# Kernel optimization log

Hardware: AMD Instinct MI355X
Metric: run time of the kernel (lower is better)

Reference implementation:

```python
import jax, jax.numpy as jnp
import numpy as np

B, S, D, F, E, CAP = 4, 2048, 1024, 4096, 8, 320


def setup_inputs() -> dict:
    key = jax.random.key(0)
    k1, k2, k3, k4 = jax.random.split(key, 4)
    return {
        "hidden_states": jax.random.normal(k1, (B, S, D), dtype=jnp.float32),
        "router_w": jax.random.normal(k2, (D, E), dtype=jnp.float32) * 0.02,
        "wi": jax.random.normal(k3, (E, D, F), dtype=jnp.float32) * 0.02,
        "wo": jax.random.normal(k4, (E, F, D), dtype=jnp.float32) * 0.02,
    }


def reference(hidden_states, router_w, wi, wo):
    # ---- Router (Switch top-1 with per-sequence expert capacity) ----
    b, s, d = hidden_states.shape
    e = router_w.shape[1]
    logits = hidden_states.astype(jnp.float32) @ router_w          # [B,S,E]
    probs = jax.nn.softmax(logits, axis=-1)                        # [B,S,E]
    expert_idx = jnp.argmax(probs, axis=-1)                        # [B,S]
    onehot = jax.nn.one_hot(expert_idx, e, dtype=jnp.int32)        # [B,S,E]
    priority = jnp.cumsum(onehot, axis=1)                          # cumsum over seq dim (dim=-2)
    keep = onehot * (priority <= CAP).astype(jnp.int32)            # capacity-masked router_mask

    # slot of each token within its chosen expert (0-based)
    slot = jnp.take_along_axis(priority, expert_idx[..., None], axis=-1)[..., 0] - 1  # [B,S]
    valid = slot < CAP                                             # dropped tokens exceed capacity
    slot_sc = jnp.where(valid, slot, CAP)                          # out-of-range -> dropped by scatter

    b_ar = jnp.broadcast_to(jnp.arange(b)[:, None], (b, s))
    s_ar = jnp.broadcast_to(jnp.arange(s)[None, :], (b, s))
    dispatch = jnp.zeros((b, e, CAP), jnp.int32).at[b_ar, expert_idx, slot_sc].set(
        s_ar.astype(jnp.int32), mode="drop")                       # [B,E,CAP] token index per slot
    slot_used = jnp.zeros((b, e, CAP), bool).at[b_ar, expert_idx, slot_sc].set(
        valid, mode="drop")                                        # [B,E,CAP]

    # ---- Dispatch: gather tokens into [B,E,CAP,D] ----
    xg = jax.vmap(lambda xb, ib: xb[ib])(hidden_states, dispatch)  # [B,E,CAP,D]

    # ---- Per-expert dense FFN (grouped GEMM) ----
    hg = jax.nn.relu(jnp.einsum("becd,edf->becf", xg, wi))         # [B,E,CAP,F]
    yg = jnp.einsum("becf,efd->becd", hg, wo)                      # [B,E,CAP,D]

    # ---- Combine: scatter expert outputs back; unrouted tokens keep input ----
    idx_back = jnp.where(slot_used, dispatch, s)                   # out-of-range -> dropped
    next_states = jax.vmap(
        lambda xb, ib, yb: xb.at[ib.reshape(-1)].set(yb.reshape(-1, d), mode="drop")
    )(hidden_states, idx_back, yg)                                 # [B,S,D]

    max_prob = jnp.max(probs, axis=-1, keepdims=True)              # [B,S,1]
    out = max_prob * next_states
    expert_index_out = jnp.argmax(keep, axis=-1)                   # [B,S] (0 for dropped tokens)
    return out, logits, expert_index_out
```

## Files before the change

### kernel.cpp

```cpp
#include <hip/hip_runtime.h>
#include <hip/hip_bf16.h>
#include <stdint.h>

#define B_ 4
#define S_ 2048
#define D_ 1024
#define F_ 4096
#define E_ 8
#define CAP_ 320
#define BS_ (B_*S_)
#define MPE 1280

typedef unsigned short u16;
typedef __attribute__((ext_vector_type(8))) short bf16x8;
typedef __attribute__((ext_vector_type(4))) float f32x4;
typedef __attribute__((ext_vector_type(4))) unsigned short u16x4;
typedef __attribute__((ext_vector_type(8))) unsigned short u16x8;

__device__ __forceinline__ u16 f2bf(float f) {
  union { float f; uint32_t u; } v; v.f = f;
  uint32_t r = (v.u + 0x7FFFu + ((v.u >> 16) & 1u)) >> 16;
  return (u16)r;
}

__device__ __forceinline__ void gload16(const void* g, void* l) {
  __builtin_amdgcn_global_load_lds(
      (const __attribute__((address_space(1))) uint32_t*)g,
      (__attribute__((address_space(3))) uint32_t*)l, 16, 0, 0);
}

__device__ __forceinline__ void transpose_block(
    const float* __restrict__ W, u16* __restrict__ WT,
    const int K, const int N, const int bid, void* ldsraw)
{
  float (*tile)[65] = (float(*)[65])ldsraw;
  const int tk = K >> 7, tn = N >> 6;
  const int e = bid / (tk * tn), r = bid % (tk * tn);
  const int k0 = (r / tn) << 7, n0 = (r % tn) << 6;
  const float* We = W + (size_t)e * K * N;
  u16* WTe = WT + (size_t)e * N * K;
  const int t = threadIdx.x;
  const int fr = t >> 2, c0 = (t & 3) * 16;
#pragma unroll
  for (int j = 0; j < 4; ++j) {
    const float4 v = *(const float4*)(We + (size_t)(k0 + fr) * N + n0 + c0 + j * 4);
    tile[fr][c0 + j*4 + 0] = v.x; tile[fr][c0 + j*4 + 1] = v.y;
    tile[fr][c0 + j*4 + 2] = v.z; tile[fr][c0 + j*4 + 3] = v.w;
  }
  __syncthreads();
  const int nr = t >> 3, kk0 = (t & 7) * 16;
  u16x8 o0, o1;
#pragma unroll
  for (int j = 0; j < 8; ++j) o0[j] = f2bf(tile[kk0 + j][nr]);
#pragma unroll
  for (int j = 0; j < 8; ++j) o1[j] = f2bf(tile[kk0 + 8 + j][nr]);
  u16* dst = WTe + (size_t)(n0 + nr) * K + k0 + kk0;
  *(u16x8*)dst = o0;
  *(u16x8*)(dst + 8) = o1;
}

__global__ __launch_bounds__(512) void transpose_kernel(
    const float* __restrict__ W, u16* __restrict__ WT, const int K, const int N)
{
  __shared__ __align__(16) float tile[128][65];
  transpose_block(W, WT, K, N, blockIdx.x, (void*)tile);
}

__global__ __launch_bounds__(512) void prep_kernel(
    const float* __restrict__ hs, const float* __restrict__ rw,
    const float* __restrict__ wi, u16* __restrict__ wT,
    float* __restrict__ logits, float* __restrict__ maxp,
    int* __restrict__ eidx, const int twiT)
{
  __shared__ __align__(16) float tile[128][65];
  if ((int)blockIdx.x < twiT) {
    transpose_block(wi, wT, D_, F_, blockIdx.x, (void*)tile);
    return;
  }
  const int wv = threadIdx.x >> 6, l = threadIdx.x & 63;
  const int token = (blockIdx.x - twiT) * 8 + wv;
  const float* row = hs + (size_t)token * D_;
  const float4* rw4 = (const float4*)rw;

  double acc0=0, acc1=0, acc2=0, acc3=0, acc4=0, acc5=0, acc6=0, acc7=0;
#pragma unroll
  for (int j = 0; j < 4; ++j) {
    const int d4 = l + j * 64;
    const float4 v = ((const float4*)row)[d4];
#pragma unroll
    for (int c = 0; c < 4; ++c) {
      const int d = d4 * 4 + c;
      const float x = (&v.x)[c];
      const float4 w0 = rw4[d * 2];
      const float4 w1 = rw4[d * 2 + 1];
      acc0 += (double)x * (double)w0.x;
      acc1 += (double)x * (double)w0.y;
      acc2 += (double)x * (double)w0.z;
      acc3 += (double)x * (double)w0.w;
      acc4 += (double)x * (double)w1.x;
      acc5 += (double)x * (double)w1.y;
      acc6 += (double)x * (double)w1.z;
      acc7 += (double)x * (double)w1.w;
    }
  }
  double acc[E_] = {acc0, acc1, acc2, acc3, acc4, acc5, acc6, acc7};
#pragma unroll
  for (int e = 0; e < E_; ++e) {
#pragma unroll
    for (int off = 32; off; off >>= 1)
      acc[e] += __shfl_xor(acc[e], off);
  }
  if (l == 0) {
    float lg[E_];
#pragma unroll
    for (int e = 0; e < E_; ++e) lg[e] = (float)acc[e];
    float lmax = lg[0]; int am = 0;
#pragma unroll
    for (int e = 1; e < E_; ++e) { if (lg[e] > lmax) { lmax = lg[e]; am = e; } }
    float sum = 0.f;
#pragma unroll
    for (int e = 0; e < E_; ++e) sum += expf(lg[e] - lmax);
#pragma unroll
    for (int e = 0; e < E_; ++e) logits[(size_t)token * E_ + e] = lg[e];
    maxp[token] = 1.0f / sum;
    eidx[token] = am;
  }
}

__global__ __launch_bounds__(256) void scan_kernel(
    const int* __restrict__ eidx, int* __restrict__ tok,
    float* __restrict__ eout, const float* __restrict__ hs,
    const float* __restrict__ maxp, float* __restrict__ out)
{
  const int b = blockIdx.x >> 3, e = blockIdx.x & 7;
  __shared__ int wsum[4];
  const int tid = threadIdx.x, wv = tid >> 6, l = tid & 63;
  for (int i = tid; i < CAP_; i += 256) tok[(b * E_ + e) * CAP_ + i] = -1;
  __syncthreads();
  int base = 0;
  for (int ch = 0; ch < S_ / 256; ++ch) {
    const int s = ch * 256 + tid;
    const bool p = (eidx[b * S_ + s] == e);
    const unsigned long long m = __ballot(p);
    const int lp = __popcll(m & ((1ULL << l) - 1ULL));
    if (l == 0) wsum[wv] = __popcll(m);
    __syncthreads();
    int pre = 0, tot = 0;
#pragma unroll
    for (int w = 0; w < 4; ++w) { if (w < wv) pre += wsum[w]; tot += wsum[w]; }
    if (p) {
      const int rank = base + pre + lp;
      if (rank < CAP_) {
        tok[(b * E_ + e) * CAP_ + rank] = s;
        eout[b * S_ + s] = (float)e;
      } else {
        eout[b * S_ + s] = 0.0f;
        const float mp = maxp[b * S_ + s];
        const float4* src = (const float4*)(hs + (size_t)(b * S_ + s) * D_);
        float4* dst = (float4*)(out + (size_t)(b * S_ + s) * D_);
        for (int j = 0; j < D_ / 4; ++j) {
          const float4 vv = src[j];
          float4 o; o.x = vv.x * mp; o.y = vv.y * mp; o.z = vv.z * mp; o.w = vv.w * mp;
          dst[j] = o;
        }
      }
    }
    base += tot;
    __syncthreads();
  }
}

__global__ __launch_bounds__(256) void gather_kernel(
    const float* __restrict__ hs, const int* __restrict__ tok,
    u16* __restrict__ Xg)
{
  const int bx = blockIdx.x;
  const int e = bx / MPE, r = bx % MPE;
  const int b = r / CAP_, c = r % CAP_;
  const int t = tok[(b * E_ + e) * CAP_ + c];
  const int d = threadIdx.x * 4;
  u16x4 o;
  if (t >= 0) {
    const float4 vv = *(const float4*)(hs + ((size_t)(b * S_ + t)) * D_ + d);
    o[0] = f2bf(vv.x); o[1] = f2bf(vv.y); o[2] = f2bf(vv.z); o[3] = f2bf(vv.w);
  } else {
    o[0] = 0; o[1] = 0; o[2] = 0; o[3] = 0;
  }
  *(u16x4*)(Xg + (size_t)bx * D_ + d) = o;
}

#define BAR() __builtin_amdgcn_s_barrier()
#define LGKMN(n) do { asm volatile("s_waitcnt lgkmcnt(" #n ")" ::: "memory"); \
                      __builtin_amdgcn_sched_barrier(0); } while (0)
#define VMW(n) asm volatile("s_waitcnt vmcnt(" #n ")" ::: "memory")

__global__ __launch_bounds__(512, 2) void moe_g1(
    const u16* __restrict__ Aall, const u16* __restrict__ Btall,
    u16* __restrict__ hgout, const int gemm_blocks,
    const float* __restrict__ Wtr, u16* __restrict__ WTtr)
{
  __shared__ __align__(16) u16 lds[49152];

#define LDA(p, h) (lds + (p) * 8192 + (h) * 4096)
#define LDB(p, h) (lds + 16384 + (p) * 16384 + (h) * 8192)

  if ((int)blockIdx.x >= gemm_blocks) {
    transpose_block(Wtr, WTtr, F_, D_, blockIdx.x - gemm_blocks, (void*)lds);
    return;
  }
  const int K = D_, NT = K >> 6, N = F_;
  const int cpx = gemm_blocks >> 3;
  const int bid = blockIdx.x;
  const int swzb = (bid & 7) * cpx + (bid >> 3);
  const int e = swzb / 160, rem = swzb % 160;
  const int m0 = (rem / 16) * 128, n0 = (rem % 16) * 256;

  const u16* Ae = Aall + (size_t)e * MPE * K;
  const u16* Be = Btall + (size_t)e * N * K;

  const int tid = threadIdx.x;
  const int wv = tid >> 6, l = tid & 63;
  const int wr = wv >> 2, wc = wv & 3;
  const int lr = l & 15, lk = l >> 4;
  const int rswz = ((lr >> 3) & 1) << 4;
  const int gs0 = tid ^ (((tid >> 5) & 1) << 1);
  const size_t goffB = (size_t)((gs0 >> 2) & 127) * K + (size_t)((gs0 & 3) * 8);
  const size_t goffA = (size_t)((gs0 >> 2) & 63) * K
                     + (size_t)(((gs0 >> 8) & 1) * 32) + (size_t)((gs0 & 3) * 8);
  const int dwoff = wv * 512;

  const u16* pA0 = Ae + (size_t)m0 * K;
  const u16* pA1 = Ae + (size_t)(m0 + 64) * K;
  const u16* pB0 = Be + (size_t)n0 * K;
  const u16* pB1 = Be + (size_t)(n0 + 128) * K;

  f32x4 acc[4][4];
#pragma unroll
  for (int i = 0; i < 4; ++i)
#pragma unroll
    for (int j = 0; j < 4; ++j) acc[i][j] = (f32x4){0.f, 0.f, 0.f, 0.f};

  bf16x8 faA[2], faB[2], fb[8];

#define STAGE_A1(dhalf, rb, tt) \
    gload16((rb) + goffA + (size_t)((tt) * 64), (dhalf) + dwoff)

#define STAGE_B1(dhalf, rb, tt) do {                                       \
    const u16* s_ = (rb) + goffB + (size_t)((tt) * 64);                    \
    gload16(s_,      (dhalf) + dwoff);                                     \
    gload16(s_ + 32, (dhalf) + 4096 + dwoff);                              \
  } while (0)

#define READ_AQ1(q, p, fa_) do {                                           \
    _Pragma("unroll")                                                      \
    for (int kk = 0; kk < 2; ++kk)                                         \
      fa_[kk] = *(const bf16x8*)&LDA(p, wr)                                \
          [(kk*64 + (q)*16 + lr)*32 + ((lk*8) ^ rswz)];                    \
  } while (0)

#define READ_B_ALL1(p) do {                                                \
    _Pragma("unroll")                                                      \
    for (int nf = 0; nf < 4; ++nf)                                         \
      _Pragma("unroll")                                                    \
      for (int kk = 0; kk < 2; ++kk)                                       \
        fb[nf*2+kk] = *(const bf16x8*)&LDB(p, wc>>1)                       \
            [(kk*128 + (wc&1)*64 + (nf>>1)*32 + (nf&1)*16 + lr)*32         \
             + ((lk*8) ^ rswz)];                                           \
  } while (0)

#define MFMA_P1(q, fa_) do {                                               \
    __builtin_amdgcn_s_setprio(1);                                         \
    _Pragma("unroll")                                                      \
    for (int nf = 0; nf < 4; ++nf)                                         \
      _Pragma("unroll")                                                    \
      for (int kk = 0; kk < 2; ++kk)                                       \
        acc[q][nf] = __builtin_amdgcn_mfma_f32_16x16x32_bf16(              \
            fa_[kk], fb[nf*2+kk], acc[q][nf], 0, 0, 0);                    \
    __builtin_amdgcn_s_setprio(0);                                         \
  } while (0)

#define DO_T1(p, pn, tc) do {                                              \
    READ_AQ1(1, p, faB);                                                   \
    if ((tc) + 1 < NT) { STAGE_A1(LDA(pn,0), pA0, (tc)+1);                 \
                         STAGE_A1(LDA(pn,1), pA1, (tc)+1); }               \
    LGKMN(2); MFMA_P1(0, faA);                                             \
    READ_AQ1(2, p, faA);                                                   \
    LGKMN(2); MFMA_P1(1, faB);                                             \
    BAR();                                                                 \
    READ_AQ1(3, p, faB);                                                   \
    if ((tc) + 2 < NT) { STAGE_B1(LDB(p,0), pB0, (tc)+2);                  \
                         STAGE_B1(LDB(p,1), pB1, (tc)+2); }                \
    LGKMN(2); MFMA_P1(2, faA);                                             \
    LGKMN(0); MFMA_P1(3, faB);                                             \
    if ((tc) >= NT - 2) VMW(0); else VMW(4);                               \
    BAR();                                                                 \
    if ((tc) + 1 < NT) { READ_B_ALL1(pn); READ_AQ1(0, pn, faA); }          \
  } while (0)

  STAGE_A1(LDA(0,0), pA0, 0);
  STAGE_A1(LDA(0,1), pA1, 0);
  STAGE_B1(LDB(0,0), pB0, 0);
  STAGE_B1(LDB(0,1), pB1, 0);
  STAGE_B1(LDB(1,0), pB0, 1);
  STAGE_B1(LDB(1,1), pB1, 1);
  VMW(4); BAR();
  READ_B_ALL1(0); READ_AQ1(0, 0, faA);

  for (int t = 0; t < NT; t += 2) {
    DO_T1(0, 1, t);
    DO_T1(1, 0, t + 1);
  }

#pragma unroll
  for (int i = 0; i < 4; ++i) {
#pragma unroll
    for (int r = 0; r < 4; ++r) {
      const int grow = m0 + wr * 64 + i * 16 + lk * 4 + r;
      u16* hrow = hgout + ((size_t)e * MPE + grow) * (size_t)N + n0 + wc * 64;
#pragma unroll
      for (int j = 0; j < 4; ++j)
        hrow[j * 16 + lr] = f2bf(fmaxf(acc[i][j][r], 0.0f));
    }
  }
#undef LDA
#undef LDB
#undef STAGE_A1
#undef STAGE_B1
#undef READ_AQ1
#undef READ_B_ALL1
#undef MFMA_P1
#undef DO_T1
}

__global__ __launch_bounds__(512, 2) void moe_g2(
    const u16* __restrict__ Aall, const u16* __restrict__ Btall,
    float* __restrict__ out, const int* __restrict__ tok,
    const float* __restrict__ maxp)
{
  __shared__ __align__(16) u16 lds[2][2][2][8192];

  const int K = F_, NT = K >> 6, N = D_;
  const int gemm_blocks = 160, cpx = gemm_blocks >> 3;
  const int bid = blockIdx.x;
  const int swzb = (bid & 7) * cpx + (bid >> 3);
  const int e = swzb / 20, rem = swzb % 20;
  const int m0 = (rem / 4) * 256, n0 = (rem % 4) * 256;

  const u16* Ae = Aall + (size_t)e * MPE * K;
  const u16* Be = Btall + (size_t)e * N * K;

  const int tid = threadIdx.x;
  const int wv = tid >> 6, l = tid & 63;
  const int wr = wv >> 2, wc = wv & 3;
  const int lr = l & 15, lk = l >> 4;
  const int rswz = ((lr >> 3) & 1) << 4;
  const int gs0 = tid ^ (((tid >> 5) & 1) << 1);
  const size_t goff = (size_t)((gs0 >> 2) & 127) * K + (size_t)((gs0 & 3) * 8);
  const int dwoff = wv * 512;

  const u16* pA0 = Ae + (size_t)m0 * K;
  const u16* pA1 = Ae + (size_t)(m0 + 128) * K;
  const u16* pB0 = Be + (size_t)n0 * K;
  const u16* pB1 = Be + (size_t)(n0 + 128) * K;

  f32x4 acc[8][4];
#pragma unroll
  for (int i = 0; i < 8; ++i)
#pragma unroll
    for (int j = 0; j < 4; ++j) acc[i][j] = (f32x4){0.f, 0.f, 0.f, 0.f};

  bf16x8 faA[4], faB[4], fb[8];

#define LDSH(p, ab, h) (&lds[p][ab][h][0])

#define STAGE2(dhalf, rb, tt) do {                                         \
    const u16* s_ = (rb) + goff + (size_t)((tt) * 64);                     \
    gload16(s_,      (dhalf) + dwoff);                                     \
    gload16(s_ + 32, (dhalf) + 4096 + dwoff);                              \
  } while (0)

#define READ_AQ2(q, p, fa_) do {                                           \
    _Pragma("unroll")                                                      \
    for (int mf = 0; mf < 2; ++mf)                                         \
      _Pragma("unroll")                                                    \
      for (int kk = 0; kk < 2; ++kk)                                       \
        fa_[mf*2+kk] = *(const bf16x8*)&lds[p][0][wr]                      \
            [(kk*128 + (q)*32 + mf*16 + lr)*32 + ((lk*8) ^ rswz)];         \
  } while (0)

#define READ_B_ALL2(p) do {                                                \
    _Pragma("unroll")                                                      \
    for (int nf = 0; nf < 4; ++nf)                                         \
      _Pragma("unroll")                                                    \
      for (int kk = 0; kk < 2; ++kk)                                       \
        fb[nf*2+kk] = *(const bf16x8*)&lds[p][1][wc>>1]                    \
            [(kk*128 + (wc&1)*64 + (nf>>1)*32 + (nf&1)*16 + lr)*32         \
             + ((lk*8) ^ rswz)];                                           \
  } while (0)

#define MFMA_P2(q, fa_) do {                                               \
    __builtin_amdgcn_s_setprio(1);                                         \
    _Pragma("unroll")                                                      \
    for (int mf = 0; mf < 2; ++mf)                                         \
      _Pragma("unroll")                                                    \
      for (int nf = 0; nf < 4; ++nf)                                       \
        _Pragma("unroll")                                                  \
        for (int kk = 0; kk < 2; ++kk)                                     \
          acc[(q)*2+mf][nf] = __builtin_amdgcn_mfma_f32_16x16x32_bf16(     \
              fa_[mf*2+kk], fb[nf*2+kk], acc[(q)*2+mf][nf], 0, 0, 0);      \
    __builtin_amdgcn_s_setprio(0);                                         \
  } while (0)

#define DO_T2(p, pn, tc) do {                                              \
    READ_AQ2(1, p, faB);                                                   \
    if ((tc) + 1 < NT) { STAGE2(LDSH(pn,0,0), pA0, (tc)+1);                \
                         STAGE2(LDSH(pn,0,1), pA1, (tc)+1); }              \
    LGKMN(4); MFMA_P2(0, faA);                                             \
    READ_AQ2(2, p, faA);                                                   \
    LGKMN(4); MFMA_P2(1, faB);                                             \
    BAR();                                                                 \
    READ_AQ2(3, p, faB);                                                   \
    if ((tc) + 2 < NT) { STAGE2(LDSH(p,1,0), pB0, (tc)+2);                 \
                         STAGE2(LDSH(p,1,1), pB1, (tc)+2); }               \
    LGKMN(4); MFMA_P2(2, faA);                                             \
    LGKMN(0); MFMA_P2(3, faB);                                             \
    if ((tc) >= NT - 2) VMW(0); else VMW(4);                               \
    BAR();                                                                 \
    if ((tc) + 1 < NT) { READ_B_ALL2(pn); READ_AQ2(0, pn, faA); }          \
  } while (0)

  STAGE2(LDSH(0,0,0), pA0, 0);
  STAGE2(LDSH(0,0,1), pA1, 0);
  STAGE2(LDSH(0,1,0), pB0, 0);
  STAGE2(LDSH(0,1,1), pB1, 0);
  STAGE2(LDSH(1,1,0), pB0, 1);
  STAGE2(LDSH(1,1,1), pB1, 1);
  VMW(4); BAR();
  READ_B_ALL2(0); READ_AQ2(0, 0, faA);

  for (int t = 0; t < NT; t += 2) {
    DO_T2(0, 1, t);
    DO_T2(1, 0, t + 1);
  }

#pragma unroll
  for (int i = 0; i < 8; ++i) {
#pragma unroll
    for (int r = 0; r < 4; ++r) {
      const int grow = m0 + wr * 128 + i * 16 + lk * 4 + r;
      const int b = grow / CAP_, c = grow % CAP_;
      const int t = tok[(b * E_ + e) * CAP_ + c];
      if (t >= 0) {
        const float sc = maxp[b * S_ + t];
        float* orow = out + ((size_t)(b * S_ + t)) * D_ + n0 + wc * 64;
#pragma unroll
        for (int j = 0; j < 4; ++j)
          orow[j * 16 + lr] = sc * acc[i][j][r];
      }
    }
  }
#undef LDSH
#undef STAGE2
#undef READ_AQ2
#undef READ_B_ALL2
#undef MFMA_P2
#undef DO_T2
}

extern "C" void kernel_launch(void* const* d_in, const int* in_sizes, int n_in,
                              void* d_out, int out_size, void* d_ws, size_t ws_size,
                              hipStream_t stream)
{
  const float* hs = (const float*)d_in[0];
  const float* rw = (const float*)d_in[1];
  const float* wi = (const float*)d_in[2];
  const float* wo = (const float*)d_in[3];

  float* out    = (float*)d_out;
  float* logits = out + (size_t)BS_ * D_;
  float* eout   = logits + (size_t)BS_ * E_;

  uint8_t* ws = (uint8_t*)d_ws;
  int*   tok  = (int*)(ws + 0);
  float* maxp = (float*)(ws + 40960);
  int*   eidx = (int*)(ws + 73728);
  u16*   Xg   = (u16*)(ws + 131072);
  u16*   hg   = (u16*)(ws + 21102592);
  u16*   wiT  = (u16*)(ws + 104988672);
  if (ws_size < 172097536ULL) return;
  const bool big = ws_size >= 239206400ULL;
  u16* woT = big ? (u16*)(ws + 172097536) : wiT;

  const int twiT = E_ * (D_ / 128) * (F_ / 64);
  const int twoT = E_ * (F_ / 128) * (D_ / 64);
  const int g1 = E_ * (MPE / 128) * (F_ / 256);
  const int g2 = 160;

  prep_kernel<<<twiT + BS_ / 8, 512, 0, stream>>>(
      hs, rw, wi, wiT, logits, maxp, eidx, twiT);
  scan_kernel<<<B_ * E_, 256, 0, stream>>>(eidx, tok, eout, hs, maxp, out);
  gather_kernel<<<E_ * MPE, 256, 0, stream>>>(hs, tok, Xg);

  if (big) {
    moe_g1<<<g1 + twoT, 512, 0, stream>>>(Xg, wiT, hg, g1, wo, woT);
  } else {
    moe_g1<<<g1, 512, 0, stream>>>(Xg, wiT, hg, g1, nullptr, nullptr);
    transpose_kernel<<<twoT, 512, 0, stream>>>(wo, woT, F_, D_);
  }
  moe_g2<<<g2, 512, 0, stream>>>(hg, woT, out, tok, maxp);
}
```

Measured before the change: 330.6 us.

## Retile second expert GEMM to 320x128 tiles aligned to per-batch capacity

Changes the second grouped GEMM from 256x256 tiles (160 blocks) to 320x128 tiles (256 blocks), so each M tile is exactly one batch's capacity slice and the batch index becomes constant per block. The LDS layout, staging, fragment reads, MFMA chunking and epilogue are rewritten for 10 row fragments by 2 column fragments per wave. The aim is to fill more of the device's compute units than 160 blocks did and to make the output scatter simpler. In exchange each tile has lower arithmetic intensity, larger LDS use, and launch bounds that allow only one block per CU.

```diff
diff --git a/kernel.cpp b/kernel.cpp
--- a/kernel.cpp
+++ b/kernel.cpp
@@ -332,22 +332,23 @@
 #undef DO_T1
 }
 
-__global__ __launch_bounds__(512, 2) void moe_g2(
+__global__ __launch_bounds__(512, 1) void moe_g2(
     const u16* __restrict__ Aall, const u16* __restrict__ Btall,
     float* __restrict__ out, const int* __restrict__ tok,
     const float* __restrict__ maxp)
 {
-  __shared__ __align__(16) u16 lds[2][2][2][8192];
-
-  const int K = F_, NT = K >> 6, N = D_;
-  const int gemm_blocks = 160, cpx = gemm_blocks >> 3;
+  __shared__ __align__(16) u16 ldsA[2][20480];
+  __shared__ __align__(16) u16 ldsB[2][8192];
+
+  const int K = F_, NT = K >> 6;
   const int bid = blockIdx.x;
-  const int swzb = (bid & 7) * cpx + (bid >> 3);
-  const int e = swzb / 20, rem = swzb % 20;
-  const int m0 = (rem / 4) * 256, n0 = (rem % 4) * 256;
-
-  const u16* Ae = Aall + (size_t)e * MPE * K;
-  const u16* Be = Btall + (size_t)e * N * K;
+  const int swzb = (bid & 7) * 32 + (bid >> 3);
+  const int e = swzb >> 5, rem = swzb & 31;
+  const int m0 = (rem >> 3) * 320, n0 = (rem & 7) * 128;
+  const int b = m0 / CAP_;
+
+  const u16* pA = Aall + (size_t)e * MPE * K + (size_t)m0 * K;
+  const u16* pB = Btall + (size_t)e * D_ * K + (size_t)n0 * K;
 
   const int tid = threadIdx.x;
   const int wv = tid >> 6, l = tid & 63;
@@ -356,54 +357,60 @@
   const int rswz = ((lr >> 3) & 1) << 4;
   const int gs0 = tid ^ (((tid >> 5) & 1) << 1);
   const size_t goff = (size_t)((gs0 >> 2) & 127) * K + (size_t)((gs0 & 3) * 8);
+  const size_t goffR = (size_t)(256 + ((gs0 >> 2) & 63)) * K + (size_t)((gs0 & 3) * 8);
   const int dwoff = wv * 512;
-
-  const u16* pA0 = Ae + (size_t)m0 * K;
-  const u16* pA1 = Ae + (size_t)(m0 + 128) * K;
-  const u16* pB0 = Be + (size_t)n0 * K;
-  const u16* pB1 = Be + (size_t)(n0 + 128) * K;
-
-  f32x4 acc[8][4];
-#pragma unroll
-  for (int i = 0; i < 8; ++i)
-#pragma unroll
-    for (int j = 0; j < 4; ++j) acc[i][j] = (f32x4){0.f, 0.f, 0.f, 0.f};
-
-  bf16x8 faA[4], faB[4], fb[8];
-
-#define LDSH(p, ab, h) (&lds[p][ab][h][0])
-
-#define STAGE2(dhalf, rb, tt) do {                                         \
-    const u16* s_ = (rb) + goff + (size_t)((tt) * 64);                     \
-    gload16(s_,      (dhalf) + dwoff);                                     \
-    gload16(s_ + 32, (dhalf) + 4096 + dwoff);                              \
-  } while (0)
-
-#define READ_AQ2(q, p, fa_) do {                                           \
+  const int dwoff4 = (wv & 3) * 512;
+  const size_t r128K = (size_t)128 * K;
+
+  f32x4 acc[10][2];
+#pragma unroll
+  for (int i = 0; i < 10; ++i)
+#pragma unroll
+    for (int j = 0; j < 2; ++j) acc[i][j] = (f32x4){0.f, 0.f, 0.f, 0.f};
+
+  bf16x8 faA[4], faB[4], fb[4];
+
+#define STAGE_A2(p, tt) do {                                               \
+    const u16* s_ = pA + goff + (size_t)((tt) * 64);                       \
+    gload16(s_,             &ldsA[p][0]     + dwoff);                      \
+    gload16(s_ + r128K,     &ldsA[p][4096]  + dwoff);                      \
+    gload16(s_ + 32,        &ldsA[p][10240] + dwoff);                      \
+    gload16(s_ + r128K + 32,&ldsA[p][14336] + dwoff);                      \
+    const u16* sR = pA + goffR + (size_t)((tt) * 64);                      \
+    if (wv < 4) gload16(sR,      &ldsA[p][8192]  + dwoff4);                \
+    else        gload16(sR + 32, &ldsA[p][18432] + dwoff4);                \
+  } while (0)
+
+#define STAGE_B2(p, tt) do {                                               \
+    const u16* s_ = pB + goff + (size_t)((tt) * 64);                       \
+    gload16(s_,      &ldsB[p][0]    + dwoff);                              \
+    gload16(s_ + 32, &ldsB[p][4096] + dwoff);                              \
+  } while (0)
+
+#define READ_CH2(q, p, fa_) do {                                           \
     _Pragma("unroll")                                                      \
     for (int mf = 0; mf < 2; ++mf)                                         \
       _Pragma("unroll")                                                    \
       for (int kk = 0; kk < 2; ++kk)                                       \
-        fa_[mf*2+kk] = *(const bf16x8*)&lds[p][0][wr]                      \
-            [(kk*128 + (q)*32 + mf*16 + lr)*32 + ((lk*8) ^ rswz)];         \
+        fa_[mf*2+kk] = *(const bf16x8*)&ldsA[p]                            \
+            [(kk*320 + wr*160 + ((q)*2+mf)*16 + lr)*32 + ((lk*8) ^ rswz)]; \
   } while (0)
 
 #define READ_B_ALL2(p) do {                                                \
     _Pragma("unroll")                                                      \
-    for (int nf = 0; nf < 4; ++nf)                                         \
+    for (int nf = 0; nf < 2; ++nf)                                         \
       _Pragma("unroll")                                                    \
       for (int kk = 0; kk < 2; ++kk)                                       \
-        fb[nf*2+kk] = *(const bf16x8*)&lds[p][1][wc>>1]                    \
-            [(kk*128 + (wc&1)*64 + (nf>>1)*32 + (nf&1)*16 + lr)*32         \
-             + ((lk*8) ^ rswz)];                                           \
-  } while (0)
-
-#define MFMA_P2(q, fa_) do {                                               \
+        fb[nf*2+kk] = *(const bf16x8*)&ldsB[p]                             \
+            [(kk*128 + wc*32 + nf*16 + lr)*32 + ((lk*8) ^ rswz)];          \
+  } while (0)
+
+#define MFMA_CH2(q, fa_) do {                                              \
     __builtin_amdgcn_s_setprio(1);                                         \
     _Pragma("unroll")                                                      \
     for (int mf = 0; mf < 2; ++mf)                                         \
       _Pragma("unroll")                                                    \
-      for (int nf = 0; nf < 4; ++nf)                                       \
+      for (int nf = 0; nf < 2; ++nf)                                       \
         _Pragma("unroll")                                                  \
         for (int kk = 0; kk < 2; ++kk)                                     \
           acc[(q)*2+mf][nf] = __builtin_amdgcn_mfma_f32_16x16x32_bf16(     \
@@ -411,59 +418,54 @@
     __builtin_amdgcn_s_setprio(0);                                         \
   } while (0)
 
-#define DO_T2(p, pn, tc) do {                                              \
-    READ_AQ2(1, p, faB);                                                   \
-    if ((tc) + 1 < NT) { STAGE2(LDSH(pn,0,0), pA0, (tc)+1);                \
-                         STAGE2(LDSH(pn,0,1), pA1, (tc)+1); }              \
-    LGKMN(4); MFMA_P2(0, faA);                                             \
-    READ_AQ2(2, p, faA);                                                   \
-    LGKMN(4); MFMA_P2(1, faB);                                             \
+#define DO_T2(p, pn, tc, fE, fO) do {                                      \
+    READ_CH2(1, p, fO);                                                    \
+    if ((tc) + 1 < NT) STAGE_A2(pn, (tc) + 1);                             \
+    LGKMN(4); MFMA_CH2(0, fE);                                             \
+    READ_CH2(2, p, fE);                                                    \
+    LGKMN(4); MFMA_CH2(1, fO);                                             \
     BAR();                                                                 \
-    READ_AQ2(3, p, faB);                                                   \
-    if ((tc) + 2 < NT) { STAGE2(LDSH(p,1,0), pB0, (tc)+2);                 \
-                         STAGE2(LDSH(p,1,1), pB1, (tc)+2); }               \
-    LGKMN(4); MFMA_P2(2, faA);                                             \
-    LGKMN(0); MFMA_P2(3, faB);                                             \
-    if ((tc) >= NT - 2) VMW(0); else VMW(4);                               \
+    READ_CH2(3, p, fO);                                                    \
+    if ((tc) + 2 < NT) STAGE_B2(p, (tc) + 2);                              \
+    LGKMN(4); MFMA_CH2(2, fE);                                             \
+    READ_CH2(4, p, fE);                                                    \
+    LGKMN(4); MFMA_CH2(3, fO);                                             \
+    LGKMN(0); MFMA_CH2(4, fE);                                             \
+    if ((tc) >= NT - 2) VMW(0); else VMW(2);                               \
     BAR();                                                                 \
-    if ((tc) + 1 < NT) { READ_B_ALL2(pn); READ_AQ2(0, pn, faA); }          \
-  } while (0)
-
-  STAGE2(LDSH(0,0,0), pA0, 0);
-  STAGE2(LDSH(0,0,1), pA1, 0);
-  STAGE2(LDSH(0,1,0), pB0, 0);
-  STAGE2(LDSH(0,1,1), pB1, 0);
-  STAGE2(LDSH(1,1,0), pB0, 1);
-  STAGE2(LDSH(1,1,1), pB1, 1);
-  VMW(4); BAR();
-  READ_B_ALL2(0); READ_AQ2(0, 0, faA);
+    if ((tc) + 1 < NT) { READ_B_ALL2(pn); READ_CH2(0, pn, fO); }           \
+  } while (0)
+
+  STAGE_A2(0, 0);
+  STAGE_B2(0, 0);
+  STAGE_B2(1, 1);
+  VMW(2); BAR();
+  READ_B_ALL2(0); READ_CH2(0, 0, faA);
 
   for (int t = 0; t < NT; t += 2) {
-    DO_T2(0, 1, t);
-    DO_T2(1, 0, t + 1);
-  }
-
-#pragma unroll
-  for (int i = 0; i < 8; ++i) {
+    DO_T2(0, 1, t,     faA, faB);
+    DO_T2(1, 0, t + 1, faB, faA);
+  }
+
+#pragma unroll
+  for (int i = 0; i < 10; ++i) {
 #pragma unroll
     for (int r = 0; r < 4; ++r) {
-      const int grow = m0 + wr * 128 + i * 16 + lk * 4 + r;
-      const int b = grow / CAP_, c = grow % CAP_;
+      const int c = wr * 160 + i * 16 + lk * 4 + r;
       const int t = tok[(b * E_ + e) * CAP_ + c];
       if (t >= 0) {
         const float sc = maxp[b * S_ + t];
-        float* orow = out + ((size_t)(b * S_ + t)) * D_ + n0 + wc * 64;
-#pragma unroll
-        for (int j = 0; j < 4; ++j)
-          orow[j * 16 + lr] = sc * acc[i][j][r];
+        float* orow = out + ((size_t)(b * S_ + t)) * D_ + n0 + wc * 32;
+        orow[lr]      = sc * acc[i][0][r];
+        orow[16 + lr] = sc * acc[i][1][r];
       }
     }
   }
-#undef LDSH
-#undef STAGE2
-#undef READ_AQ2
+#undef STAGE_A2
+#undef STAGE_B2
+#undef READ_CH2
 #undef READ_B_ALL2
-#undef MFMA_P2
+#undef MFMA_CH2
 #undef DO_T2
 }
 
@@ -494,7 +496,7 @@
   const int twiT = E_ * (D_ / 128) * (F_ / 64);
   const int twoT = E_ * (F_ / 128) * (D_ / 64);
   const int g1 = E_ * (MPE / 128) * (F_ / 256);
-  const int g2 = 160;
+  const int g2 = 256;
 
   prep_kernel<<<twiT + BS_ / 8, 512, 0, stream>>>(
       hs, rw, wi, wiT, logits, maxp, eidx, twiT);
```

Result: slower. 359.7 us (+8.8%).
